# Kernel optimization log

Hardware: AMD Instinct MI355X
Metric: run time of the kernel (lower is better)

The kernel has to match this reference:

```python
import jax, jax.numpy as jnp
import numpy as np

IN_DIM = 128
MEM = 128
BRANCH = 8
DEPTH = 6
N = (BRANCH ** (DEPTH + 1) - 1) // (BRANCH - 1)  # 299593 nodes, BFS order


def setup_inputs() -> dict:
    key = jax.random.key(0)
    ks = jax.random.split(key, 9)
    s_in = 1.0 / np.sqrt(IN_DIM)
    s_m = 1.0 / np.sqrt(MEM)
    f32 = jnp.float32
    return {
        "x": jax.random.normal(ks[0], (N, IN_DIM), f32),
        "W_ioux": jax.random.normal(ks[1], (3 * MEM, IN_DIM), f32) * s_in,
        "b_ioux": jax.random.normal(ks[2], (3 * MEM,), f32) * s_in,
        "W_iouh": jax.random.normal(ks[3], (3 * MEM, MEM), f32) * s_m,
        "b_iouh": jax.random.normal(ks[4], (3 * MEM,), f32) * s_m,
        "W_fx": jax.random.normal(ks[5], (MEM, IN_DIM), f32) * s_in,
        "b_fx": jax.random.normal(ks[6], (MEM,), f32) * s_in,
        "W_fh": jax.random.normal(ks[7], (MEM, MEM), f32) * s_m,
        "b_fh": jax.random.normal(ks[8], (MEM,), f32) * s_m,
        "branch": BRANCH,
        "depth": DEPTH,
    }


def reference(x, W_ioux, b_ioux, W_iouh, b_iouh, W_fx, b_fx, W_fh, b_fh, branch, depth):
    """Child-Sum TreeLSTM over a complete `branch`-ary tree of `depth` levels.

    Nodes are stored in BFS order: level l occupies [off(l), off(l+1)) and the
    children of local parent p at level l are contiguous at level l+1, so the
    recursion becomes a bottom-up sweep with one batched step per level.
    Matches torch node_forward exactly (leaf nodes see a single zero child row,
    i.e. h_sum = 0 -> iouh contributes only its bias, and fc_sum = 0).
    """
    mem = W_fh.shape[0]
    off = lambda l: (branch ** l - 1) // (branch - 1)
    c_prev = h_prev = None  # states of level l+1, [branch**(l+1), mem]
    for l in range(depth, -1, -1):
        n_l = branch ** l
        x_l = x[off(l): off(l) + n_l]  # [n_l, in_dim]
        if l == depth:  # leaves
            h_sum = jnp.zeros((n_l, mem), x.dtype)
            fc_sum = jnp.zeros((n_l, mem), x.dtype)
        else:
            c_ch = c_prev.reshape(n_l, branch, mem)
            h_ch = h_prev.reshape(n_l, branch, mem)
            h_sum = h_ch.sum(axis=1)  # child-sum of h
            # per-child forget gate: sigmoid(fh(h_child) + fx(x_parent))
            f = jax.nn.sigmoid(
                jnp.einsum('nbm,km->nbk', h_ch, W_fh) + b_fh
                + (x_l @ W_fx.T + b_fx)[:, None, :]
            )
            fc_sum = (f * c_ch).sum(axis=1)
        iou = x_l @ W_ioux.T + b_ioux + h_sum @ W_iouh.T + b_iouh
        i, o, u = jnp.split(iou, 3, axis=1)
        c_prev = jax.nn.sigmoid(i) * jnp.tanh(u) + fc_sum
        h_prev = jax.nn.sigmoid(o) * jnp.tanh(c_prev)
    return (c_prev, h_prev)  # root state, each [1, mem]
```

## Files before the change

kernel.cpp:

```cpp
#include <hip/hip_runtime.h>
#include <hip/hip_bf16.h>

#define TB 256
#define LOG2E  1.44269504088896f
#define LOG2E2 2.88539008177793f

typedef __attribute__((ext_vector_type(8))) short bf16x8;
typedef __attribute__((ext_vector_type(4))) float f32x4;

__device__ __forceinline__ unsigned pk2(float a, float b){
  float2 t; t.x = a; t.y = b;
  __hip_bfloat162 h = __float22bfloat162_rn(t);
  union { __hip_bfloat162 h; unsigned u; } cv; cv.h = h; return cv.u;
}
__device__ __forceinline__ bf16x8 cvt8(float4 a, float4 b){
  union { unsigned u[4]; bf16x8 v; } r;
  r.u[0] = pk2(a.x, a.y); r.u[1] = pk2(a.z, a.w);
  r.u[2] = pk2(b.x, b.y); r.u[3] = pk2(b.z, b.w);
  return r.v;
}
__device__ __forceinline__ float sig2(float arg){
  return __builtin_amdgcn_rcpf(1.f + __builtin_amdgcn_exp2f(arg));
}
__device__ __forceinline__ float tanh2(float arg){
  return 1.f - 2.f*__builtin_amdgcn_rcpf(1.f + __builtin_amdgcn_exp2f(arg));
}

#define GLD16(gp, lp) __builtin_amdgcn_global_load_lds( \
    (const __attribute__((address_space(1))) void*)(gp), \
    (__attribute__((address_space(3))) void*)(lp), 16, 0, 0)

__global__ __launch_bounds__(TB)
void k_prep(const float* __restrict__ Wioux, const float* __restrict__ Wiouh,
            const float* __restrict__ Wfx,   const float* __restrict__ Wfh,
            const float* __restrict__ bioux, const float* __restrict__ biouh,
            short* __restrict__ WxG, short* __restrict__ WhG,
            short* __restrict__ WfxP, short* __restrict__ WfhP,
            float* __restrict__ biasS){
  const int q = blockIdx.x*TB + threadIdx.x;
  const int t = q >> 8, rem = q & 255;
  const int kf = rem >> 6, lane = rem & 63;
  const int row = t*16 + (lane & 15);
  const int col = kf*32 + (lane >> 4)*8;
  const size_t src = (size_t)row*128 + col;
  if (q < 6144){
    const int g = t & 7, kind = t >> 3;
    const size_t dst = ((size_t)(g*3 + kind)*4 + kf)*512 + (size_t)lane*8;
    const float4* p  = (const float4*)(Wioux + src);
    *(bf16x8*)(WxG + dst) = cvt8(p[0], p[1]);
    const float4* p2 = (const float4*)(Wiouh + src);
    *(bf16x8*)(WhG + dst) = cvt8(p2[0], p2[1]);
  }
  if (q < 2048){
    const size_t dst = ((size_t)t*4 + kf)*512 + (size_t)lane*8;
    const float4* p  = (const float4*)(Wfx + src);
    *(bf16x8*)(WfxP + dst) = cvt8(p[0], p[1]);
    const float4* p2 = (const float4*)(Wfh + src);
    *(bf16x8*)(WfhP + dst) = cvt8(p2[0], p2[1]);
  }
  if (q < 384){
    const float s = (q < 256) ? -LOG2E : LOG2E2;
    biasS[q] = s*(bioux[q] + biouh[q]);
  }
}

__global__ __launch_bounds__(TB, 4)
void k_fx(const float* __restrict__ x, const short* __restrict__ WfxP,
          const float* __restrict__ bfx, const float* __restrict__ bfh,
          float* __restrict__ FXS, int nrows){
  const int tid = threadIdx.x, wave = tid >> 6, lane = tid & 63;
  const int l15 = lane & 15, lhi = lane >> 4;
  const int mrow = (blockIdx.x*4 + wave)*16;
  const int arow = min(mrow + l15, nrows - 1);
  bf16x8 ax[4];
  const float* rp = x + (size_t)arow*128;
  #pragma unroll
  for (int kf = 0; kf < 4; ++kf){
    const float4* p = (const float4*)(rp + kf*32 + lhi*8);
    ax[kf] = cvt8(p[0], p[1]);
  }
  #pragma unroll
  for (int t = 0; t < 8; ++t){
    f32x4 acc = {0.f,0.f,0.f,0.f};
    #pragma unroll
    for (int kf = 0; kf < 4; ++kf){
      bf16x8 b = *(const bf16x8*)(WfxP + ((size_t)(t*4 + kf)*64 + lane)*8);
      acc = __builtin_amdgcn_mfma_f32_16x16x32_bf16(ax[kf], b, acc, 0,0,0);
    }
    const int col = t*16 + l15;
    const float bc = bfx[col] + bfh[col];
    #pragma unroll
    for (int r = 0; r < 4; ++r){
      const int row = mrow + lhi*4 + r;
      if (row < nrows) FXS[(size_t)row*128 + col] = -LOG2E*(acc[r] + bc);
    }
  }
}

__global__ __launch_bounds__(TB, 4)
void k_leaf(const float* __restrict__ x, int xoff,
            const short* __restrict__ WxG, const short* __restrict__ WfhP,
            const float* __restrict__ biasS, const float* __restrict__ FXS,
            int poff, short* __restrict__ HSout, float* __restrict__ FCout)
{
  __shared__ __align__(16) short wbuf[2][6144];
  __shared__ __align__(16) short hbuf[4][2048];
  const int tid = threadIdx.x;
  const int wave = tid >> 6, lane = tid & 63;
  const int l15 = lane & 15, lhi = lane >> 4;
  const int mrow = (blockIdx.x*4 + wave)*16;

  bf16x8 ax[4];
  {
    const float* rp = x + (size_t)(xoff + mrow + l15)*128;
    #pragma unroll
    for (int kf = 0; kf < 4; ++kf){
      const float4* p = (const float4*)(rp + kf*32 + lhi*8);
      ax[kf] = cvt8(p[0], p[1]);
    }
  }

  #define STAGE_L(g, b) { \
    _Pragma("unroll") \
    for (int c = 0; c < 3; ++c){ \
      const int ch = c*4 + wave; \
      GLD16(WxG + (size_t)(g)*6144 + ch*512 + lane*8, &wbuf[b][ch*512]); \
    } }

  STAGE_L(0, 0);

  float cv[8][4];
  const int p = (mrow >> 3) + (lhi >> 1);
  const float* fxp = FXS + (size_t)(poff + p)*128 + l15;
  char* hbw = (char*)hbuf[wave];

  #pragma unroll
  for (int tt = 0; tt < 8; ++tt){
    __syncthreads();
    if (tt < 7) STAGE_L(tt+1, (tt+1)&1);
    const short* wb = wbuf[tt & 1];

    f32x4 ai = {0.f,0.f,0.f,0.f}, ao = ai, au = ai;
    #pragma unroll
    for (int kf = 0; kf < 4; ++kf){
      bf16x8 bi = *(const bf16x8*)(wb + 0*2048 + kf*512 + lane*8);
      bf16x8 bo = *(const bf16x8*)(wb + 1*2048 + kf*512 + lane*8);
      bf16x8 bu = *(const bf16x8*)(wb + 2*2048 + kf*512 + lane*8);
      ai = __builtin_amdgcn_mfma_f32_16x16x32_bf16(ax[kf], bi, ai, 0,0,0);
      ao = __builtin_amdgcn_mfma_f32_16x16x32_bf16(ax[kf], bo, ao, 0,0,0);
      au = __builtin_amdgcn_mfma_f32_16x16x32_bf16(ax[kf], bu, au, 0,0,0);
    }

    const int col = tt*16 + l15;
    const float bis = biasS[col], bos = biasS[128 + col], bus = biasS[256 + col];
    float hv[4];
    float hs = 0.f;
    #pragma unroll
    for (int r = 0; r < 4; ++r){
      const float iv = sig2 (__builtin_fmaf(ai[r], -LOG2E, bis));
      const float uv = tanh2(__builtin_fmaf(au[r],  LOG2E2, bus));
      const float ov = sig2 (__builtin_fmaf(ao[r], -LOG2E, bos));
      const float c  = iv*uv;
      const float h  = ov*tanh2(LOG2E2*c);
      cv[tt][r] = c;
      hv[r] = h;
      hs += h;
    }
    const unsigned hp01 = pk2(hv[0], hv[1]);
    const unsigned hp23 = pk2(hv[2], hv[3]);
    const int cx = col*2;
    const int r0 = lhi*4;
    *(short*)(hbw + (r0  )*256 + (cx ^ ((r0  ) << 4))) = (short)hp01;
    *(short*)(hbw + (r0+1)*256 + (cx ^ ((r0+1) << 4))) = (short)(hp01 >> 16);
    *(short*)(hbw + (r0+2)*256 + (cx ^ ((r0+2) << 4))) = (short)hp23;
    *(short*)(hbw + (r0+3)*256 + (cx ^ ((r0+3) << 4))) = (short)(hp23 >> 16);

    hs += __shfl_xor(hs, 16);
    if ((lhi & 1) == 0) HSout[(size_t)p*128 + col] = (short)pk2(hs, hs);
  }

  bf16x8 af[4];
  #pragma unroll
  for (int kf = 0; kf < 4; ++kf){
    const int byte = l15*256 + (((kf*32 + lhi*8)*2) ^ (l15 << 4));
    af[kf] = *(const bf16x8*)((const char*)hbw + byte);
  }
  #pragma unroll
  for (int t2 = 0; t2 < 8; ++t2){
    f32x4 fa = {0.f,0.f,0.f,0.f};
    #pragma unroll
    for (int kf = 0; kf < 4; ++kf){
      bf16x8 b = *(const bf16x8*)(WfhP + ((size_t)(t2*4 + kf)*64 + lane)*8);
      fa = __builtin_amdgcn_mfma_f32_16x16x32_bf16(af[kf], b, fa, 0,0,0);
    }
    const float fxv = fxp[t2*16];
    float fs = 0.f;
    #pragma unroll
    for (int r = 0; r < 4; ++r){
      const float f = sig2(__builtin_fmaf(fa[r], -LOG2E, fxv));
      fs += f * cv[t2][r];
    }
    fs += __shfl_xor(fs, 16);
    if ((lhi & 1) == 0) FCout[(size_t)p*128 + t2*16 + l15] = fs;
  }
  #undef STAGE_L
}

__global__ __launch_bounds__(TB, 3)
void k_node(const float* __restrict__ x, int xoff,
            const short* __restrict__ HSin, const float* __restrict__ FCin,
            const short* __restrict__ WxG, const short* __restrict__ WhG,
            const short* __restrict__ WfhP,
            const float* __restrict__ biasS, const float* __restrict__ FXS,
            int poff, short* __restrict__ HSout, float* __restrict__ FCout,
            int nnodes)
{
  __shared__ __align__(16) short wbuf[2][12288];
  const int tid = threadIdx.x;
  const int wave = tid >> 6, lane = tid & 63;
  const int l15 = lane & 15, lhi = lane >> 4;
  const int mrow = (blockIdx.x*4 + wave)*16;
  const int arow = min(mrow + l15, nnodes - 1);

  bf16x8 ax[4], ah[4];
  {
    const float* rp = x + (size_t)(xoff + arow)*128;
    #pragma unroll
    for (int kf = 0; kf < 4; ++kf){
      const float4* p = (const float4*)(rp + kf*32 + lhi*8);
      ax[kf] = cvt8(p[0], p[1]);
    }
    const short* hp = HSin + (size_t)arow*128;
    #pragma unroll
    for (int kf = 0; kf < 4; ++kf)
      ah[kf] = *(const bf16x8*)(hp + kf*32 + lhi*8);
  }

  #define STAGE_N(g, b) { \
    _Pragma("unroll") \
    for (int c = 0; c < 3; ++c){ \
      const int ch = c*4 + wave; \
      GLD16(WxG + (size_t)(g)*6144 + ch*512 + lane*8, &wbuf[b][ch*512]); \
      GLD16(WhG + (size_t)(g)*6144 + ch*512 + lane*8, &wbuf[b][6144 + ch*512]); \
    } }

  STAGE_N(0, 0);

  float cv[8][4];
  unsigned hpk[8][2];
  const int p = (mrow >> 3) + (lhi >> 1);
  const float* fxp = FXS + (size_t)(poff + p)*128 + l15;

  #pragma unroll
  for (int tt = 0; tt < 8; ++tt){
    __syncthreads();
    if (tt < 7) STAGE_N(tt+1, (tt+1)&1);
    const short* wb = wbuf[tt & 1];

    f32x4 ai = {0.f,0.f,0.f,0.f}, ao = ai, au = ai;
    #pragma unroll
    for (int kf = 0; kf < 4; ++kf){
      bf16x8 bi = *(const bf16x8*)(wb + 0*2048 + kf*512 + lane*8);
      bf16x8 bo = *(const bf16x8*)(wb + 1*2048 + kf*512 + lane*8);
      bf16x8 bu = *(const bf16x8*)(wb + 2*2048 + kf*512 + lane*8);
      ai = __builtin_amdgcn_mfma_f32_16x16x32_bf16(ax[kf], bi, ai, 0,0,0);
      ao = __builtin_amdgcn_mfma_f32_16x16x32_bf16(ax[kf], bo, ao, 0,0,0);
      au = __builtin_amdgcn_mfma_f32_16x16x32_bf16(ax[kf], bu, au, 0,0,0);
    }
    #pragma unroll
    for (int kf = 0; kf < 4; ++kf){
      bf16x8 bi = *(const bf16x8*)(wb + 6144 + 0*2048 + kf*512 + lane*8);
      bf16x8 bo = *(const bf16x8*)(wb + 6144 + 1*2048 + kf*512 + lane*8);
      bf16x8 bu = *(const bf16x8*)(wb + 6144 + 2*2048 + kf*512 + lane*8);
      ai = __builtin_amdgcn_mfma_f32_16x16x32_bf16(ah[kf], bi, ai, 0,0,0);
      ao = __builtin_amdgcn_mfma_f32_16x16x32_bf16(ah[kf], bo, ao, 0,0,0);
      au = __builtin_amdgcn_mfma_f32_16x16x32_bf16(ah[kf], bu, au, 0,0,0);
    }

    const int col = tt*16 + l15;
    const float bis = biasS[col], bos = biasS[128 + col], bus = biasS[256 + col];
    float hv[4];
    float hs = 0.f;
    #pragma unroll
    for (int r = 0; r < 4; ++r){
      const float fc = FCin[(size_t)(mrow + lhi*4 + r)*128 + col];
      const float iv = sig2 (__builtin_fmaf(ai[r], -LOG2E, bis));
      const float uv = tanh2(__builtin_fmaf(au[r],  LOG2E2, bus));
      const float ov = sig2 (__builtin_fmaf(ao[r], -LOG2E, bos));
      const float c  = __builtin_fmaf(iv, uv, fc);
      const float h  = ov*tanh2(LOG2E2*c);
      cv[tt][r] = c;
      hv[r] = h;
      hs += h;
    }
    hpk[tt][0] = pk2(hv[0], hv[1]);
    hpk[tt][1] = pk2(hv[2], hv[3]);
    hs += __shfl_xor(hs, 16);
    if ((lhi & 1) == 0) HSout[(size_t)p*128 + col] = (short)pk2(hs, hs);
  }

  __syncthreads();
  char* hbw = (char*)(((short*)wbuf) + wave*2048);
  #pragma unroll
  for (int t2 = 0; t2 < 8; ++t2){
    const int cx = (t2*16 + l15)*2;
    const int r0 = lhi*4;
    *(short*)(hbw + (r0  )*256 + (cx ^ ((r0  ) << 4))) = (short)hpk[t2][0];
    *(short*)(hbw + (r0+1)*256 + (cx ^ ((r0+1) << 4))) = (short)(hpk[t2][0] >> 16);
    *(short*)(hbw + (r0+2)*256 + (cx ^ ((r0+2) << 4))) = (short)hpk[t2][1];
    *(short*)(hbw + (r0+3)*256 + (cx ^ ((r0+3) << 4))) = (short)(hpk[t2][1] >> 16);
  }
  bf16x8 af[4];
  #pragma unroll
  for (int kf = 0; kf < 4; ++kf){
    const int byte = l15*256 + (((kf*32 + lhi*8)*2) ^ (l15 << 4));
    af[kf] = *(const bf16x8*)((const char*)hbw + byte);
  }
  #pragma unroll
  for (int t2 = 0; t2 < 8; ++t2){
    f32x4 fa = {0.f,0.f,0.f,0.f};
    #pragma unroll
    for (int kf = 0; kf < 4; ++kf){
      bf16x8 b = *(const bf16x8*)(WfhP + ((size_t)(t2*4 + kf)*64 + lane)*8);
      fa = __builtin_amdgcn_mfma_f32_16x16x32_bf16(af[kf], b, fa, 0,0,0);
    }
    const float fxv = fxp[t2*16];
    float fs = 0.f;
    #pragma unroll
    for (int r = 0; r < 4; ++r){
      const float f = sig2(__builtin_fmaf(fa[r], -LOG2E, fxv));
      fs += f * cv[t2][r];
    }
    fs += __shfl_xor(fs, 16);
    if ((lhi & 1) == 0) FCout[(size_t)p*128 + t2*16 + l15] = fs;
  }
  #undef STAGE_N
}

__device__ __forceinline__ void tail_level(
    const float* __restrict__ x, int xoff,
    const short* __restrict__ HSin, const float* __restrict__ FCin,
    const short* __restrict__ WxG, const short* __restrict__ WhG,
    const short* __restrict__ WfhP,
    const float* __restrict__ biasS, const float* __restrict__ FXS, int poff,
    short* __restrict__ HSout, float* __restrict__ FCout,
    float* __restrict__ dout, int nnodes, short* __restrict__ hb)
{
  const int tid = threadIdx.x;
  const int lane = tid & 63;
  const int l15 = lane & 15, lhi = lane >> 4;
  const int mrow = (tid >> 6)*16;
  const int arow = min(mrow + l15, nnodes - 1);

  bf16x8 ax[4], ah[4];
  {
    const float* rp = x + (size_t)(xoff + arow)*128;
    #pragma unroll
    for (int kf = 0; kf < 4; ++kf){
      const float4* p = (const float4*)(rp + kf*32 + lhi*8);
      ax[kf] = cvt8(p[0], p[1]);
    }
    const short* hp = HSin + (size_t)arow*128;
    #pragma unroll
    for (int kf = 0; kf < 4; ++kf)
      ah[kf] = *(const bf16x8*)(hp + kf*32 + lhi*8);
  }

  float cv[8][4];
  const int p = (min(mrow, nnodes - 1) >> 3) + (lhi >> 1);
  const float* fxp = FXS + (size_t)(poff + min(p, (nnodes - 1) >> 3))*128 + l15;

  #pragma unroll
  for (int tt = 0; tt < 8; ++tt){
    f32x4 ai = {0.f,0.f,0.f,0.f}, ao = ai, au = ai;
    #pragma unroll
    for (int kf = 0; kf < 4; ++kf){
      bf16x8 bxi = *(const bf16x8*)(WxG + ((size_t)(tt*3 + 0)*4 + kf)*512 + lane*8);
      bf16x8 bxo = *(const bf16x8*)(WxG + ((size_t)(tt*3 + 1)*4 + kf)*512 + lane*8);
      bf16x8 bxu = *(const bf16x8*)(WxG + ((size_t)(tt*3 + 2)*4 + kf)*512 + lane*8);
      ai = __builtin_amdgcn_mfma_f32_16x16x32_bf16(ax[kf], bxi, ai, 0,0,0);
      ao = __builtin_amdgcn_mfma_f32_16x16x32_bf16(ax[kf], bxo, ao, 0,0,0);
      au = __builtin_amdgcn_mfma_f32_16x16x32_bf16(ax[kf], bxu, au, 0,0,0);
      bf16x8 bhi = *(const bf16x8*)(WhG + ((size_t)(tt*3 + 0)*4 + kf)*512 + lane*8);
      bf16x8 bho = *(const bf16x8*)(WhG + ((size_t)(tt*3 + 1)*4 + kf)*512 + lane*8);
      bf16x8 bhu = *(const bf16x8*)(WhG + ((size_t)(tt*3 + 2)*4 + kf)*512 + lane*8);
      ai = __builtin_amdgcn_mfma_f32_16x16x32_bf16(ah[kf], bhi, ai, 0,0,0);
      ao = __builtin_amdgcn_mfma_f32_16x16x32_bf16(ah[kf], bho, ao, 0,0,0);
      au = __builtin_amdgcn_mfma_f32_16x16x32_bf16(ah[kf], bhu, au, 0,0,0);
    }
    const int col = tt*16 + l15;
    const float bis = biasS[col], bos = biasS[128 + col], bus = biasS[256 + col];
    float hs = 0.f;
    #pragma unroll
    for (int r = 0; r < 4; ++r){
      const int row = lhi*4 + r;
      const int loc = min(mrow + row, nnodes - 1);
      const float fc = FCin[(size_t)loc*128 + col];
      const float iv = sig2 (__builtin_fmaf(ai[r], -LOG2E, bis));
      const float uv = tanh2(__builtin_fmaf(au[r],  LOG2E2, bus));
      const float ov = sig2 (__builtin_fmaf(ao[r], -LOG2E, bos));
      const float c  = __builtin_fmaf(iv, uv, fc);
      const float h  = ov*tanh2(LOG2E2*c);
      cv[tt][r] = c;
      hs += h;
      const int byte = row*256 + ((l15*2 + tt*32) ^ (row << 4));
      *(short*)((char*)hb + byte) = (short)pk2(h, h);
      if (dout && (mrow + row) == 0){ dout[col] = c; dout[128 + col] = h; }
    }
    if (HSout){
      hs += __shfl_xor(hs, 16);
      if ((lhi & 1) == 0){
        const int pv = (lhi == 0) ? (mrow < nnodes) : (mrow + 8 < nnodes);
        if (pv) HSout[(size_t)p*128 + col] = (short)pk2(hs, hs);
      }
    }
  }
  if (!HSout) return;

  bf16x8 af[4];
  #pragma unroll
  for (int kf = 0; kf < 4; ++kf){
    const int byte = l15*256 + (((kf*32 + lhi*8)*2) ^ (l15 << 4));
    af[kf] = *(const bf16x8*)((const char*)hb + byte);
  }
  #pragma unroll
  for (int t2 = 0; t2 < 8; ++t2){
    f32x4 fa = {0.f,0.f,0.f,0.f};
    #pragma unroll
    for (int kf = 0; kf < 4; ++kf){
      bf16x8 b = *(const bf16x8*)(WfhP + ((size_t)(t2*4 + kf)*64 + lane)*8);
      fa = __builtin_amdgcn_mfma_f32_16x16x32_bf16(af[kf], b, fa, 0,0,0);
    }
    const float fxv = fxp[t2*16];
    float fs = 0.f;
    #pragma unroll
    for (int r = 0; r < 4; ++r){
      const float f = sig2(__builtin_fmaf(fa[r], -LOG2E, fxv));
      fs += f * cv[t2][r];
    }
    fs += __shfl_xor(fs, 16);
    if ((lhi & 1) == 0){
      const int pv = (lhi == 0) ? (mrow < nnodes) : (mrow + 8 < nnodes);
      if (pv) FCout[(size_t)p*128 + t2*16 + l15] = fs;
    }
  }
}

__global__ __launch_bounds__(TB, 1)
void k_tail(const float* __restrict__ x,
            const short* __restrict__ WxG, const short* __restrict__ WhG,
            const short* __restrict__ WfhP,
            const float* __restrict__ biasS, const float* __restrict__ FXS,
            short* __restrict__ HS0, short* __restrict__ HS1,
            float* __restrict__ FC0, float* __restrict__ FC1,
            float* __restrict__ dout)
{
  __shared__ __align__(16) short hbuf[4][2048];
  short* hb = hbuf[threadIdx.x >> 6];
  tail_level(x, 9, HS0, FC0, WxG, WhG, WfhP, biasS, FXS, 1, HS1, FC1, nullptr, 64, hb);
  __syncthreads();
  tail_level(x, 1, HS1, FC1, WxG, WhG, WfhP, biasS, FXS, 0, HS0, FC0, nullptr, 8, hb);
  __syncthreads();
  tail_level(x, 0, HS0, FC0, WxG, WhG, WfhP, biasS, FXS, 0, nullptr, nullptr, dout, 1, hb);
}

extern "C" void kernel_launch(void* const* d_in, const int* in_sizes, int n_in,
                              void* d_out, int out_size, void* d_ws, size_t ws_size,
                              hipStream_t stream)
{
  const float* x     = (const float*)d_in[0];
  const float* Wioux = (const float*)d_in[1];
  const float* bioux = (const float*)d_in[2];
  const float* Wiouh = (const float*)d_in[3];
  const float* biouh = (const float*)d_in[4];
  const float* Wfx   = (const float*)d_in[5];
  const float* bfx   = (const float*)d_in[6];
  const float* Wfh   = (const float*)d_in[7];
  const float* bfh   = (const float*)d_in[8];
  float* dout = (float*)d_out;

  static const int n_l[7]   = {1, 8, 64, 512, 4096, 32768, 262144};
  static const int off_l[7] = {0, 1, 9, 73, 585, 4681, 37449};

  char* base = (char*)d_ws;
  size_t off = 0;
  auto take = [&](size_t bytes)->char*{
    char* r = base + off;
    off = (off + bytes + 255) & ~(size_t)255;
    return r;
  };
  float* FXS  = (float*)take((size_t)37449*128*4);
  float* FC0  = (float*)take((size_t)32768*128*4);
  float* FC1  = (float*)take((size_t)32768*128*4);
  short* HS0  = (short*)take((size_t)32768*128*2);
  short* HS1  = (short*)take((size_t)32768*128*2);
  short* WxG  = (short*)take((size_t)24*2048*2);
  short* WhG  = (short*)take((size_t)24*2048*2);
  short* WfxP = (short*)take((size_t)8*2048*2);
  short* WfhP = (short*)take((size_t)8*2048*2);
  float* biasS= (float*)take((size_t)384*4);
  if (off > ws_size) return;

  short* HS[2] = {HS0, HS1};
  float* FC[2] = {FC0, FC1};

  k_prep<<<24, TB, 0, stream>>>(Wioux, Wiouh, Wfx, Wfh, bioux, biouh,
                                WxG, WhG, WfxP, WfhP, biasS);
  k_fx<<<(37449 + 63)/64, TB, 0, stream>>>(x, WfxP, bfx, bfh, FXS, 37449);

  k_leaf<<<262144/64, TB, 0, stream>>>(x, off_l[6], WxG, WfhP, biasS, FXS,
                                       off_l[5], HS1, FC1);

  for (int l = 5; l >= 3; --l){
    const int n = n_l[l];
    k_node<<<(n + 63)/64, TB, 0, stream>>>(
      x, off_l[l], HS[l & 1], FC[l & 1],
      WxG, WhG, WfhP, biasS, FXS,
      off_l[l-1], HS[(l & 1) ^ 1], FC[(l & 1) ^ 1], n);
  }
  k_tail<<<1, TB, 0, stream>>>(x, WxG, WhG, WfhP, biasS, FXS,
                               HS0, HS1, FC0, FC1, dout);
}
```

Baseline: 200.2 us.

## Read gate weights directly from global/L2 instead of LDS double-buffer staging

```diff
diff --git a/kernel.cpp b/kernel.cpp
--- a/kernel.cpp
+++ b/kernel.cpp
@@ -25,10 +25,6 @@
 __device__ __forceinline__ float tanh2(float arg){
   return 1.f - 2.f*__builtin_amdgcn_rcpf(1.f + __builtin_amdgcn_exp2f(arg));
 }
-
-#define GLD16(gp, lp) __builtin_amdgcn_global_load_lds( \
-    (const __attribute__((address_space(1))) void*)(gp), \
-    (__attribute__((address_space(3))) void*)(lp), 16, 0, 0)
 
 __global__ __launch_bounds__(TB)
 void k_prep(const float* __restrict__ Wioux, const float* __restrict__ Wiouh,
@@ -103,7 +99,6 @@
             const float* __restrict__ biasS, const float* __restrict__ FXS,
             int poff, short* __restrict__ HSout, float* __restrict__ FCout)
 {
-  __shared__ __align__(16) short wbuf[2][6144];
   __shared__ __align__(16) short hbuf[4][2048];
   const int tid = threadIdx.x;
   const int wave = tid >> 6, lane = tid & 63;
@@ -120,15 +115,6 @@
     }
   }
 
-  #define STAGE_L(g, b) { \
-    _Pragma("unroll") \
-    for (int c = 0; c < 3; ++c){ \
-      const int ch = c*4 + wave; \
-      GLD16(WxG + (size_t)(g)*6144 + ch*512 + lane*8, &wbuf[b][ch*512]); \
-    } }
-
-  STAGE_L(0, 0);
-
   float cv[8][4];
   const int p = (mrow >> 3) + (lhi >> 1);
   const float* fxp = FXS + (size_t)(poff + p)*128 + l15;
@@ -136,16 +122,12 @@
 
   #pragma unroll
   for (int tt = 0; tt < 8; ++tt){
-    __syncthreads();
-    if (tt < 7) STAGE_L(tt+1, (tt+1)&1);
-    const short* wb = wbuf[tt & 1];
-
     f32x4 ai = {0.f,0.f,0.f,0.f}, ao = ai, au = ai;
     #pragma unroll
     for (int kf = 0; kf < 4; ++kf){
-      bf16x8 bi = *(const bf16x8*)(wb + 0*2048 + kf*512 + lane*8);
-      bf16x8 bo = *(const bf16x8*)(wb + 1*2048 + kf*512 + lane*8);
-      bf16x8 bu = *(const bf16x8*)(wb + 2*2048 + kf*512 + lane*8);
+      bf16x8 bi = *(const bf16x8*)(WxG + ((size_t)((tt*3 + 0)*4 + kf)*64 + lane)*8);
+      bf16x8 bo = *(const bf16x8*)(WxG + ((size_t)((tt*3 + 1)*4 + kf)*64 + lane)*8);
+      bf16x8 bu = *(const bf16x8*)(WxG + ((size_t)((tt*3 + 2)*4 + kf)*64 + lane)*8);
       ai = __builtin_amdgcn_mfma_f32_16x16x32_bf16(ax[kf], bi, ai, 0,0,0);
       ao = __builtin_amdgcn_mfma_f32_16x16x32_bf16(ax[kf], bo, ao, 0,0,0);
       au = __builtin_amdgcn_mfma_f32_16x16x32_bf16(ax[kf], bu, au, 0,0,0);
@@ -203,10 +185,9 @@
     fs += __shfl_xor(fs, 16);
     if ((lhi & 1) == 0) FCout[(size_t)p*128 + t2*16 + l15] = fs;
   }
-  #undef STAGE_L
-}
-
-__global__ __launch_bounds__(TB, 3)
+}
+
+__global__ __launch_bounds__(TB, 4)
 void k_node(const float* __restrict__ x, int xoff,
             const short* __restrict__ HSin, const float* __restrict__ FCin,
             const short* __restrict__ WxG, const short* __restrict__ WhG,
@@ -215,66 +196,48 @@
             int poff, short* __restrict__ HSout, float* __restrict__ FCout,
             int nnodes)
 {
-  __shared__ __align__(16) short wbuf[2][12288];
+  __shared__ __align__(16) short hbuf[4][2048];
   const int tid = threadIdx.x;
   const int wave = tid >> 6, lane = tid & 63;
   const int l15 = lane & 15, lhi = lane >> 4;
   const int mrow = (blockIdx.x*4 + wave)*16;
-  const int arow = min(mrow + l15, nnodes - 1);
 
   bf16x8 ax[4], ah[4];
   {
-    const float* rp = x + (size_t)(xoff + arow)*128;
+    const float* rp = x + (size_t)(xoff + mrow + l15)*128;
     #pragma unroll
     for (int kf = 0; kf < 4; ++kf){
       const float4* p = (const float4*)(rp + kf*32 + lhi*8);
       ax[kf] = cvt8(p[0], p[1]);
     }
-    const short* hp = HSin + (size_t)arow*128;
+    const short* hp = HSin + (size_t)(mrow + l15)*128;
     #pragma unroll
     for (int kf = 0; kf < 4; ++kf)
       ah[kf] = *(const bf16x8*)(hp + kf*32 + lhi*8);
   }
 
-  #define STAGE_N(g, b) { \
-    _Pragma("unroll") \
-    for (int c = 0; c < 3; ++c){ \
-      const int ch = c*4 + wave; \
-      GLD16(WxG + (size_t)(g)*6144 + ch*512 + lane*8, &wbuf[b][ch*512]); \
-      GLD16(WhG + (size_t)(g)*6144 + ch*512 + lane*8, &wbuf[b][6144 + ch*512]); \
-    } }
-
-  STAGE_N(0, 0);
-
   float cv[8][4];
-  unsigned hpk[8][2];
   const int p = (mrow >> 3) + (lhi >> 1);
   const float* fxp = FXS + (size_t)(poff + p)*128 + l15;
+  char* hbw = (char*)hbuf[wave];
 
   #pragma unroll
   for (int tt = 0; tt < 8; ++tt){
-    __syncthreads();
-    if (tt < 7) STAGE_N(tt+1, (tt+1)&1);
-    const short* wb = wbuf[tt & 1];
-
     f32x4 ai = {0.f,0.f,0.f,0.f}, ao = ai, au = ai;
     #pragma unroll
     for (int kf = 0; kf < 4; ++kf){
-      bf16x8 bi = *(const bf16x8*)(wb + 0*2048 + kf*512 + lane*8);
-      bf16x8 bo = *(const bf16x8*)(wb + 1*2048 + kf*512 + lane*8);
-      bf16x8 bu = *(const bf16x8*)(wb + 2*2048 + kf*512 + lane*8);
-      ai = __builtin_amdgcn_mfma_f32_16x16x32_bf16(ax[kf], bi, ai, 0,0,0);
-      ao = __builtin_amdgcn_mfma_f32_16x16x32_bf16(ax[kf], bo, ao, 0,0,0);
-      au = __builtin_amdgcn_mfma_f32_16x16x32_bf16(ax[kf], bu, au, 0,0,0);
-    }
-    #pragma unroll
-    for (int kf = 0; kf < 4; ++kf){
-      bf16x8 bi = *(const bf16x8*)(wb + 6144 + 0*2048 + kf*512 + lane*8);
-      bf16x8 bo = *(const bf16x8*)(wb + 6144 + 1*2048 + kf*512 + lane*8);
-      bf16x8 bu = *(const bf16x8*)(wb + 6144 + 2*2048 + kf*512 + lane*8);
-      ai = __builtin_amdgcn_mfma_f32_16x16x32_bf16(ah[kf], bi, ai, 0,0,0);
-      ao = __builtin_amdgcn_mfma_f32_16x16x32_bf16(ah[kf], bo, ao, 0,0,0);
-      au = __builtin_amdgcn_mfma_f32_16x16x32_bf16(ah[kf], bu, au, 0,0,0);
+      bf16x8 bxi = *(const bf16x8*)(WxG + ((size_t)((tt*3 + 0)*4 + kf)*64 + lane)*8);
+      bf16x8 bxo = *(const bf16x8*)(WxG + ((size_t)((tt*3 + 1)*4 + kf)*64 + lane)*8);
+      bf16x8 bxu = *(const bf16x8*)(WxG + ((size_t)((tt*3 + 2)*4 + kf)*64 + lane)*8);
+      ai = __builtin_amdgcn_mfma_f32_16x16x32_bf16(ax[kf], bxi, ai, 0,0,0);
+      ao = __builtin_amdgcn_mfma_f32_16x16x32_bf16(ax[kf], bxo, ao, 0,0,0);
+      au = __builtin_amdgcn_mfma_f32_16x16x32_bf16(ax[kf], bxu, au, 0,0,0);
+      bf16x8 bhi = *(const bf16x8*)(WhG + ((size_t)((tt*3 + 0)*4 + kf)*64 + lane)*8);
+      bf16x8 bho = *(const bf16x8*)(WhG + ((size_t)((tt*3 + 1)*4 + kf)*64 + lane)*8);
+      bf16x8 bhu = *(const bf16x8*)(WhG + ((size_t)((tt*3 + 2)*4 + kf)*64 + lane)*8);
+      ai = __builtin_amdgcn_mfma_f32_16x16x32_bf16(ah[kf], bhi, ai, 0,0,0);
+      ao = __builtin_amdgcn_mfma_f32_16x16x32_bf16(ah[kf], bho, ao, 0,0,0);
+      au = __builtin_amdgcn_mfma_f32_16x16x32_bf16(ah[kf], bhu, au, 0,0,0);
     }
 
     const int col = tt*16 + l15;
@@ -293,23 +256,19 @@
       hv[r] = h;
       hs += h;
     }
-    hpk[tt][0] = pk2(hv[0], hv[1]);
-    hpk[tt][1] = pk2(hv[2], hv[3]);
+    const unsigned hp01 = pk2(hv[0], hv[1]);
+    const unsigned hp23 = pk2(hv[2], hv[3]);
+    const int cx = col*2;
+    const int r0 = lhi*4;
+    *(short*)(hbw + (r0  )*256 + (cx ^ ((r0  ) << 4))) = (short)hp01;
+    *(short*)(hbw + (r0+1)*256 + (cx ^ ((r0+1) << 4))) = (short)(hp01 >> 16);
+    *(short*)(hbw + (r0+2)*256 + (cx ^ ((r0+2) << 4))) = (short)hp23;
+    *(short*)(hbw + (r0+3)*256 + (cx ^ ((r0+3) << 4))) = (short)(hp23 >> 16);
+
     hs += __shfl_xor(hs, 16);
     if ((lhi & 1) == 0) HSout[(size_t)p*128 + col] = (short)pk2(hs, hs);
   }
 
-  __syncthreads();
-  char* hbw = (char*)(((short*)wbuf) + wave*2048);
-  #pragma unroll
-  for (int t2 = 0; t2 < 8; ++t2){
-    const int cx = (t2*16 + l15)*2;
-    const int r0 = lhi*4;
-    *(short*)(hbw + (r0  )*256 + (cx ^ ((r0  ) << 4))) = (short)hpk[t2][0];
-    *(short*)(hbw + (r0+1)*256 + (cx ^ ((r0+1) << 4))) = (short)(hpk[t2][0] >> 16);
-    *(short*)(hbw + (r0+2)*256 + (cx ^ ((r0+2) << 4))) = (short)hpk[t2][1];
-    *(short*)(hbw + (r0+3)*256 + (cx ^ ((r0+3) << 4))) = (short)(hpk[t2][1] >> 16);
-  }
   bf16x8 af[4];
   #pragma unroll
   for (int kf = 0; kf < 4; ++kf){
@@ -334,7 +293,6 @@
     fs += __shfl_xor(fs, 16);
     if ((lhi & 1) == 0) FCout[(size_t)p*128 + t2*16 + l15] = fs;
   }
-  #undef STAGE_N
 }
 
 __device__ __forceinline__ void tail_level(
@@ -375,15 +333,15 @@
     f32x4 ai = {0.f,0.f,0.f,0.f}, ao = ai, au = ai;
     #pragma unroll
     for (int kf = 0; kf < 4; ++kf){
-      bf16x8 bxi = *(const bf16x8*)(WxG + ((size_t)(tt*3 + 0)*4 + kf)*512 + lane*8);
-      bf16x8 bxo = *(const bf16x8*)(WxG + ((size_t)(tt*3 + 1)*4 + kf)*512 + lane*8);
-      bf16x8 bxu = *(const bf16x8*)(WxG + ((size_t)(tt*3 + 2)*4 + kf)*512 + lane*8);
+      bf16x8 bxi = *(const bf16x8*)(WxG + ((size_t)((tt*3 + 0)*4 + kf)*64 + lane)*8);
+      bf16x8 bxo = *(const bf16x8*)(WxG + ((size_t)((tt*3 + 1)*4 + kf)*64 + lane)*8);
+      bf16x8 bxu = *(const bf16x8*)(WxG + ((size_t)((tt*3 + 2)*4 + kf)*64 + lane)*8);
       ai = __builtin_amdgcn_mfma_f32_16x16x32_bf16(ax[kf], bxi, ai, 0,0,0);
       ao = __builtin_amdgcn_mfma_f32_16x16x32_bf16(ax[kf], bxo, ao, 0,0,0);
       au = __builtin_amdgcn_mfma_f32_16x16x32_bf16(ax[kf], bxu, au, 0,0,0);
-      bf16x8 bhi = *(const bf16x8*)(WhG + ((size_t)(tt*3 + 0)*4 + kf)*512 + lane*8);
-      bf16x8 bho = *(const bf16x8*)(WhG + ((size_t)(tt*3 + 1)*4 + kf)*512 + lane*8);
-      bf16x8 bhu = *(const bf16x8*)(WhG + ((size_t)(tt*3 + 2)*4 + kf)*512 + lane*8);
+      bf16x8 bhi = *(const bf16x8*)(WhG + ((size_t)((tt*3 + 0)*4 + kf)*64 + lane)*8);
+      bf16x8 bho = *(const bf16x8*)(WhG + ((size_t)((tt*3 + 1)*4 + kf)*64 + lane)*8);
+      bf16x8 bhu = *(const bf16x8*)(WhG + ((size_t)((tt*3 + 2)*4 + kf)*64 + lane)*8);
       ai = __builtin_amdgcn_mfma_f32_16x16x32_bf16(ah[kf], bhi, ai, 0,0,0);
       ao = __builtin_amdgcn_mfma_f32_16x16x32_bf16(ah[kf], bho, ao, 0,0,0);
       au = __builtin_amdgcn_mfma_f32_16x16x32_bf16(ah[kf], bhu, au, 0,0,0);
```

New measurement: 226.0 us. 1.13x slower.
